# Performance work log

Hardware: AMD Instinct MI355X
Metric: run time of the kernel (lower is better)

The kernel has to match this reference:

```python
import jax, jax.numpy as jnp
import numpy as np

H = 12          # num_attention_heads
D = 768         # hidden_size
R = 4           # channel_shrink_ratio
DH = D // H     # 64, attention_head_size
DL = D // R     # 192, layout hidden size
DHL = DH // R   # 16, layout head size
NEG = jnp.finfo(jnp.float32).min


def setup_inputs() -> dict:
    key = jax.random.key(0)
    ks = jax.random.split(key, 16)
    B, S = 8, 1024
    s = 0.02
    inp = {
        "hidden_states": jax.random.normal(ks[0], (B, S, D), jnp.float32),
        "layout_hidden_states": jax.random.normal(ks[1], (B, S, DL), jnp.float32),
        "attention_mask": jnp.ones((B, S), jnp.float32),
        "Wq": jax.random.normal(ks[2], (D, D), jnp.float32) * s,
        "bq": jnp.zeros((D,), jnp.float32),
        "Wk": jax.random.normal(ks[3], (D, D), jnp.float32) * s,
        "bk": jnp.zeros((D,), jnp.float32),
        "Wv": jax.random.normal(ks[4], (D, D), jnp.float32) * s,
        "bv": jnp.zeros((D,), jnp.float32),
        "Wlq": jax.random.normal(ks[5], (DL, DL), jnp.float32) * s,
        "blq": jnp.zeros((DL,), jnp.float32),
        "Wlk": jax.random.normal(ks[6], (DL, DL), jnp.float32) * s,
        "blk": jnp.zeros((DL,), jnp.float32),
        "Wlv": jax.random.normal(ks[7], (DL, DL), jnp.float32) * s,
        "blv": jnp.zeros((DL,), jnp.float32),
    }
    return inp


def _heads(x, hd):
    # [B,S,H*hd] -> [B,H,S,hd]
    B, S, _ = x.shape
    return x.reshape(B, S, H, hd).transpose(0, 2, 1, 3)


def reference(hidden_states, layout_hidden_states, attention_mask,
              Wq, bq, Wk, bk, Wv, bv, Wlq, blq, Wlk, blk, Wlv, blv):
    B, S, _ = hidden_states.shape
    q = _heads(hidden_states @ Wq.T + bq, DH)
    k = _heads(hidden_states @ Wk.T + bk, DH)
    v = _heads(hidden_states @ Wv.T + bv, DH)
    lq = _heads(layout_hidden_states @ Wlq.T + blq, DHL)
    lk = _heads(layout_hidden_states @ Wlk.T + blk, DHL)
    lv = _heads(layout_hidden_states @ Wlv.T + blv, DHL)

    scores = jnp.einsum('bhqd,bhkd->bhqk', q, k) / jnp.sqrt(jnp.float32(DH))
    lscores = jnp.einsum('bhqd,bhkd->bhqk', lq, lk) / jnp.sqrt(jnp.float32(DHL))
    fused = scores + lscores  # cross-added scores (same for both streams)

    bias = (1.0 - attention_mask)[:, None, None, :] * NEG  # [B,1,1,S]
    fused = fused + bias

    probs = jax.nn.softmax(fused, axis=-1)   # dropout disabled (p=0)

    ctx = jnp.einsum('bhqk,bhkd->bhqd', probs, v)
    ctx = ctx.transpose(0, 2, 1, 3).reshape(B, S, D)
    lctx = jnp.einsum('bhqk,bhkd->bhqd', probs, lv)
    lctx = lctx.transpose(0, 2, 1, 3).reshape(B, S, DL)
    return ctx, lctx, probs
```

## Files before the change

kernel.cpp:

```cpp
#include <hip/hip_runtime.h>

#define NH   12
#define SEQ  1024
#define NB   8
#define DCAT 96
#define DV   80

typedef __attribute__((ext_vector_type(8))) short  bf16x8;
typedef __attribute__((ext_vector_type(4))) float  f32x4;
typedef __attribute__((ext_vector_type(4))) unsigned short u16x4;

static __device__ __forceinline__ unsigned short f2bf(float x) {
    unsigned int u = __float_as_uint(x);
    u += 0x7fffu + ((u >> 16) & 1u);
    return (unsigned short)(u >> 16);
}
static __device__ __forceinline__ f32x4 fzero() {
    f32x4 z; z[0]=0.f; z[1]=0.f; z[2]=0.f; z[3]=0.f; return z;
}
static __device__ __forceinline__ unsigned int cvtpk(float lo, float hi) {
    unsigned int r;
    asm("v_cvt_pk_bf16_f32 %0, %1, %2" : "=v"(r) : "v"(lo), "v"(hi));
    return r;
}

#define GLDS16(gp, lp) __builtin_amdgcn_global_load_lds(                      \
    (const __attribute__((address_space(1))) void*)(gp),                      \
    (__attribute__((address_space(3))) void*)(lp), 16, 0, 0)

#define WAITV(nstr) asm volatile("s_waitcnt vmcnt(" nstr ")" ::: "memory")
#define SBARRIER() do {                                                       \
    __builtin_amdgcn_sched_barrier(0);                                        \
    asm volatile("" ::: "memory");                                            \
    __builtin_amdgcn_s_barrier();                                             \
    asm volatile("" ::: "memory");                                            \
    __builtin_amdgcn_sched_barrier(0);                                        \
} while (0)

__global__ __launch_bounds__(256) void cvt_all(
    const float* __restrict__ hs, const float* __restrict__ lhs,
    const float* __restrict__ Wq, const float* __restrict__ Wk, const float* __restrict__ Wv,
    const float* __restrict__ Wlq, const float* __restrict__ Wlk, const float* __restrict__ Wlv,
    unsigned short* __restrict__ hid16, unsigned short* __restrict__ lay16,
    unsigned short* __restrict__ wqkv16, unsigned short* __restrict__ wl16)
{
    int i = blockIdx.x * 256 + threadIdx.x;
    const float* src; unsigned short* dst; int off;
    if      (i < 1572864) { src = hs;  dst = hid16;           off = i; }
    else if (i < 1966080) { src = lhs; dst = lay16;           off = i - 1572864; }
    else if (i < 2113536) { src = Wq;  dst = wqkv16;          off = i - 1966080; }
    else if (i < 2260992) { src = Wk;  dst = wqkv16 + 589824; off = i - 2113536; }
    else if (i < 2408448) { src = Wv;  dst = wqkv16 + 1179648;off = i - 2260992; }
    else if (i < 2417664) { src = Wlq; dst = wl16;            off = i - 2408448; }
    else if (i < 2426880) { src = Wlk; dst = wl16 + 36864;    off = i - 2417664; }
    else if (i < 2436096) { src = Wlv; dst = wl16 + 73728;    off = i - 2426880; }
    else return;
    f32x4 v = ((const f32x4*)src)[off];
    u16x4 o;
    o[0] = f2bf(v[0]); o[1] = f2bf(v[1]); o[2] = f2bf(v[2]); o[3] = f2bf(v[3]);
    ((u16x4*)dst)[off] = o;
}

__global__ __launch_bounds__(256) void proj_gemm(
    const unsigned short* __restrict__ A,
    const unsigned short* __restrict__ Bw,
    const float* __restrict__ b0, const float* __restrict__ b1, const float* __restrict__ b2,
    unsigned short* __restrict__ Qc, unsigned short* __restrict__ Kc, unsigned short* __restrict__ VT,
    int K, int Ntot, int variant)
{
    __shared__ __align__(16) unsigned short As[4096];
    __shared__ __align__(16) unsigned short Bs[4096];
    const int tid = threadIdx.x, w = tid >> 6, lane = tid & 63;
    const int g = lane >> 4, c = lane & 15;
    const int m0 = blockIdx.x * 128, n0 = blockIdx.y * 128;
    const int wr = w >> 1, wc = w & 1;
    const int srow = lane >> 2, scol = (lane & 3) * 8;

    f32x4 acc[4][4];
    #pragma unroll
    for (int m = 0; m < 4; m++)
        #pragma unroll
        for (int n = 0; n < 4; n++) acc[m][n] = fzero();

    const int ch0 = w * 2, ch1 = w * 2 + 1;
    const size_t arow0 = (size_t)(m0 + ch0 * 16 + srow) * K + scol;
    const size_t arow1 = (size_t)(m0 + ch1 * 16 + srow) * K + scol;
    int bn0 = n0 + ch0 * 16 + srow; if (bn0 >= Ntot) bn0 = Ntot - 1;
    int bn1 = n0 + ch1 * 16 + srow; if (bn1 >= Ntot) bn1 = Ntot - 1;
    const size_t brow0 = (size_t)bn0 * K + scol;
    const size_t brow1 = (size_t)bn1 * K + scol;

    for (int k0 = 0; k0 < K; k0 += 32) {
        __syncthreads();
        GLDS16(A  + arow0 + k0, As + ch0 * 512);
        GLDS16(A  + arow1 + k0, As + ch1 * 512);
        GLDS16(Bw + brow0 + k0, Bs + ch0 * 512);
        GLDS16(Bw + brow1 + k0, Bs + ch1 * 512);
        __syncthreads();
        bf16x8 af[4], bfr[4];
        #pragma unroll
        for (int m = 0; m < 4; m++) af[m]  = *(const bf16x8*)&As[(wr*64 + m*16 + c)*32 + g*8];
        #pragma unroll
        for (int n = 0; n < 4; n++) bfr[n] = *(const bf16x8*)&Bs[(wc*64 + n*16 + c)*32 + g*8];
        #pragma unroll
        for (int m = 0; m < 4; m++)
            #pragma unroll
            for (int n = 0; n < 4; n++)
                acc[m][n] = __builtin_amdgcn_mfma_f32_16x16x32_bf16(af[m], bfr[n], acc[m][n], 0, 0, 0);
    }

    const int b_ = m0 >> 10;
    #pragma unroll
    for (int nf = 0; nf < 4; nf++) {
        int n = n0 + wc * 64 + nf * 16 + c;
        if (n >= Ntot) continue;
        int seg, nn;
        if (variant == 0) { seg = (n >= 1536) ? 2 : ((n >= 768) ? 1 : 0); nn = n - seg * 768; }
        else              { seg = (n >= 384)  ? 2 : ((n >= 192) ? 1 : 0); nn = n - seg * 192; }
        const float* bp = (seg == 0) ? b0 : ((seg == 1) ? b1 : b2);
        float bv = bp[nn];
        float scale = (seg == 0) ? (variant ? 0.25f : 0.125f) : 1.0f;
        int h, d;
        if (variant == 0) { h = nn >> 6; d = nn & 63; }
        else              { h = nn >> 4; d = 64 + (nn & 15); }
        #pragma unroll
        for (int m = 0; m < 4; m++) {
            int row = m0 + wr * 64 + m * 16 + 4 * g;
            int s = row & 1023;
            if (seg < 2) {
                unsigned short* dst = (seg == 0) ? Qc : Kc;
                size_t base = (size_t)(b_ * NH + h) * SEQ;
                #pragma unroll
                for (int r = 0; r < 4; r++) {
                    dst[(base + s + r) * DCAT + d] = f2bf((acc[m][nf][r] + bv) * scale);
                    if (variant == 1)
                        dst[(base + s + r) * DCAT + d + 16] = 0;
                }
            } else {
                u16x4 pk;
                #pragma unroll
                for (int r = 0; r < 4; r++) pk[r] = f2bf(acc[m][nf][r] + bv);
                int kb = s >> 5, ko = s & 31;
                *(u16x4*)&VT[(((size_t)(b_ * NH + h) * 32 + kb) * DV + d) * 32 + ko] = pk;
            }
        }
    }
}

__global__ __launch_bounds__(256, 3) void attn_kernel(
    const unsigned short* __restrict__ Qc,
    const unsigned short* __restrict__ Kc,
    const unsigned short* __restrict__ VT,
    const float* __restrict__ mask,
    float* __restrict__ ctx,
    float* __restrict__ lctx,
    float* __restrict__ probs)
{
    __shared__ __align__(16) unsigned short Ks[2 * 6144];
    __shared__ __align__(16) unsigned short pbuf[4][32][36];

    const int tid = threadIdx.x, w = tid >> 6, lane = tid & 63;
    const int g = lane >> 4, c = lane & 15;

    const int bid = blockIdx.x;
    const int xc = bid & 7, j = bid >> 3;
    const int bh = xc + 8 * (j >> 3);
    const int qt = j & 7;
    const int b = bh / NH, h = bh % NH;
    const int qrb = qt * 128 + w * 32;
    const float NEGF = -3.4028234663852886e38f;

    bf16x8 qa0, qa1, qa2, qb0, qb1, qb2;
    {
        const unsigned short* qr0 = &Qc[((size_t)bh * SEQ + qrb + c) * DCAT + g * 8];
        qa0 = *(const bf16x8*)(qr0);
        qa1 = *(const bf16x8*)(qr0 + 32);
        qa2 = *(const bf16x8*)(qr0 + 64);
        const unsigned short* qr1 = qr0 + 16 * DCAT;
        qb0 = *(const bf16x8*)(qr1);
        qb1 = *(const bf16x8*)(qr1 + 32);
        qb2 = *(const bf16x8*)(qr1 + 64);
    }
    const unsigned short* Kb = Kc + (size_t)bh * SEQ * DCAT;
    const unsigned short* Vb = VT + (size_t)bh * 32 * DV * 32;
    const float* mk = mask + b * SEQ;

    const int slot8 = (g ^ ((c >> 1) & 3)) * 8;

    const unsigned short* gsrc[3]; int gstep[3];
    #pragma unroll
    for (int r = 0; r < 3; r++) {
        const int m = tid + 256 * r;
        if (m < 384) {
            int p = m >> 7, row = (m >> 2) & 31, jj = m & 3;
            int jx = jj ^ ((row >> 1) & 3);
            gsrc[r]  = Kb + row * DCAT + p * 32 + jx * 8;
            gstep[r] = 32 * DCAT;
        } else if (m < 704) {
            int mv = m - 384;
            int df = mv >> 6, cc = (mv >> 2) & 15, jj = mv & 3;
            int jx = jj ^ ((cc >> 1) & 3);
            gsrc[r]  = Vb + (df * 16 + cc) * 32 + jx * 8;
            gstep[r] = DV * 32;
        } else {
            gsrc[r]  = Vb;
            gstep[r] = 0;
        }
    }
    const int dub = w * 512;

    f32x4 cacc0[5], cacc1[5];
    #pragma unroll
    for (int nf = 0; nf < 5; nf++) { cacc0[nf] = fzero(); cacc1[nf] = fzero(); }
    float sm0 = 0.f, sm1 = 0.f;

    #pragma unroll
    for (int r = 0; r < 3; r++)
        GLDS16(gsrc[r], Ks + r * 2048 + dub);
    __builtin_amdgcn_sched_barrier(0);

    for (int t = 0; t < 32; t++) {
        const int buf = t & 1;
        if (t == 0) WAITV("0");
        else        WAITV("2");
        SBARRIER();
        if (t < 31) {
            #pragma unroll
            for (int r = 0; r < 3; r++)
                GLDS16(gsrc[r] + (t + 1) * gstep[r], Ks + (buf ^ 1) * 6144 + r * 2048 + dub);
            __builtin_amdgcn_sched_barrier(0);
        }

        #pragma unroll
        for (int ktl = 0; ktl < 2; ktl++) {
            const int rb = buf * 6144 + (ktl * 16 + c) * 32 + slot8;
            bf16x8 k0 = *(const bf16x8*)&Ks[rb];
            bf16x8 k1 = *(const bf16x8*)&Ks[rb + 1024];
            bf16x8 k2 = *(const bf16x8*)&Ks[rb + 2048];
            f32x4 m4 = *(const f32x4*)&mk[t * 32 + ktl * 16 + 4 * g];
            __builtin_amdgcn_s_setprio(1);
            f32x4 a0 = __builtin_amdgcn_mfma_f32_16x16x32_bf16(k0, qa0, fzero(), 0, 0, 0);
            f32x4 a1 = __builtin_amdgcn_mfma_f32_16x16x32_bf16(k1, qa1, fzero(), 0, 0, 0);
            f32x4 a2 = __builtin_amdgcn_mfma_f32_16x16x32_bf16(k2, qa2, fzero(), 0, 0, 0);
            f32x4 b0 = __builtin_amdgcn_mfma_f32_16x16x32_bf16(k0, qb0, fzero(), 0, 0, 0);
            f32x4 b1 = __builtin_amdgcn_mfma_f32_16x16x32_bf16(k1, qb1, fzero(), 0, 0, 0);
            f32x4 b2 = __builtin_amdgcn_mfma_f32_16x16x32_bf16(k2, qb2, fzero(), 0, 0, 0);
            __builtin_amdgcn_s_setprio(0);
            f32x4 e0, e1;
            #pragma unroll
            for (int r = 0; r < 4; r++) {
                float bias = (1.0f - m4[r]) * NEGF;
                e0[r] = __expf(a0[r] + a1[r] + a2[r] + bias);
                e1[r] = __expf(b0[r] + b1[r] + b2[r] + bias);
                sm0 += e0[r];
                sm1 += e1[r];
            }
            uint2 hh0, hh1;
            hh0.x = cvtpk(e0[0], e0[1]); hh0.y = cvtpk(e0[2], e0[3]);
            hh1.x = cvtpk(e1[0], e1[1]); hh1.y = cvtpk(e1[2], e1[3]);
            *(uint2*)&pbuf[w][c][ktl * 16 + 4 * g]      = hh0;
            *(uint2*)&pbuf[w][16 + c][ktl * 16 + 4 * g] = hh1;
        }
        const int vb0 = buf * 6144 + 3072 + c * 32 + slot8;
        bf16x8 vf0 = *(const bf16x8*)&Ks[vb0];
        bf16x8 vf1 = *(const bf16x8*)&Ks[vb0 + 512];
        bf16x8 vf2 = *(const bf16x8*)&Ks[vb0 + 1024];
        bf16x8 vf3 = *(const bf16x8*)&Ks[vb0 + 1536];
        bf16x8 vf4 = *(const bf16x8*)&Ks[vb0 + 2048];
        bf16x8 pa0 = *(const bf16x8*)&pbuf[w][c][g * 8];
        bf16x8 pa1 = *(const bf16x8*)&pbuf[w][16 + c][g * 8];
        __builtin_amdgcn_s_setprio(1);
        cacc0[0] = __builtin_amdgcn_mfma_f32_16x16x32_bf16(pa0, vf0, cacc0[0], 0, 0, 0);
        cacc1[0] = __builtin_amdgcn_mfma_f32_16x16x32_bf16(pa1, vf0, cacc1[0], 0, 0, 0);
        cacc0[1] = __builtin_amdgcn_mfma_f32_16x16x32_bf16(pa0, vf1, cacc0[1], 0, 0, 0);
        cacc1[1] = __builtin_amdgcn_mfma_f32_16x16x32_bf16(pa1, vf1, cacc1[1], 0, 0, 0);
        cacc0[2] = __builtin_amdgcn_mfma_f32_16x16x32_bf16(pa0, vf2, cacc0[2], 0, 0, 0);
        cacc1[2] = __builtin_amdgcn_mfma_f32_16x16x32_bf16(pa1, vf2, cacc1[2], 0, 0, 0);
        cacc0[3] = __builtin_amdgcn_mfma_f32_16x16x32_bf16(pa0, vf3, cacc0[3], 0, 0, 0);
        cacc1[3] = __builtin_amdgcn_mfma_f32_16x16x32_bf16(pa1, vf3, cacc1[3], 0, 0, 0);
        cacc0[4] = __builtin_amdgcn_mfma_f32_16x16x32_bf16(pa0, vf4, cacc0[4], 0, 0, 0);
        cacc1[4] = __builtin_amdgcn_mfma_f32_16x16x32_bf16(pa1, vf4, cacc1[4], 0, 0, 0);
        __builtin_amdgcn_s_setprio(0);
    }

    sm0 += __shfl_xor(sm0, 16); sm0 += __shfl_xor(sm0, 32);
    sm1 += __shfl_xor(sm1, 16); sm1 += __shfl_xor(sm1, 32);
    const float rinv0 = 1.0f / fmaxf(sm0, 1e-38f);
    const float rinv1 = 1.0f / fmaxf(sm1, 1e-38f);

    float rl0[4], rl1[4];
    #pragma unroll
    for (int r = 0; r < 4; r++) {
        rl0[r] = __shfl(rinv0, 4 * g + r);
        rl1[r] = __shfl(rinv1, 4 * g + r);
    }

    #pragma unroll
    for (int nf = 0; nf < 4; nf++)
        #pragma unroll
        for (int r = 0; r < 4; r++) {
            int q0 = qrb + 4 * g + r;
            ctx[((size_t)(b * SEQ + q0)) * 768 + h * 64 + nf * 16 + c] = cacc0[nf][r] * rl0[r];
            ctx[((size_t)(b * SEQ + q0 + 16)) * 768 + h * 64 + nf * 16 + c] = cacc1[nf][r] * rl1[r];
        }
    #pragma unroll
    for (int r = 0; r < 4; r++) {
        int q0 = qrb + 4 * g + r;
        lctx[((size_t)(b * SEQ + q0)) * 192 + h * 16 + c] = cacc0[4][r] * rl0[r];
        lctx[((size_t)(b * SEQ + q0 + 16)) * 192 + h * 16 + c] = cacc1[4][r] * rl1[r];
    }

    const int srow   = lane >> 2;
    const int schunk = (lane & 3) ^ ((lane >> 3) & 3);
    const int ssrcA  = (w * 16 + srow) * DCAT + schunk * 8;
    unsigned short* sdstA = &Ks[w * 512];

    const size_t prow0 = ((size_t)bh * SEQ + qrb + c) * SEQ;
    const size_t prow1 = prow0 + 16 * SEQ;

    SBARRIER();
    #pragma unroll
    for (int p = 0; p < 3; p++) GLDS16(Kb + ssrcA + p * 32, sdstA + p * 2048);
    __builtin_amdgcn_sched_barrier(0);

    for (int t = 0; t < 16; t++) {
        const int buf = t & 1;
        if (t == 0) WAITV("0");
        else        WAITV("12");
        SBARRIER();
        if (t < 15) {
            const unsigned short* src = Kb + (t + 1) * 6144 + ssrcA;
            unsigned short* dst = sdstA + (buf ^ 1) * 6144;
            #pragma unroll
            for (int p = 0; p < 3; p++) GLDS16(src + p * 32, dst + p * 2048);
            __builtin_amdgcn_sched_barrier(0);
        }
        #pragma unroll
        for (int ktl = 0; ktl < 4; ktl++) {
            const int rb = buf * 6144 + (ktl * 16 + c) * 32 + slot8;
            bf16x8 k0 = *(const bf16x8*)&Ks[rb];
            bf16x8 k1 = *(const bf16x8*)&Ks[rb + 2048];
            bf16x8 k2 = *(const bf16x8*)&Ks[rb + 4096];
            f32x4 m4 = *(const f32x4*)&mk[t * 64 + ktl * 16 + 4 * g];
            __builtin_amdgcn_s_setprio(1);
            f32x4 a0 = __builtin_amdgcn_mfma_f32_16x16x32_bf16(k0, qa0, fzero(), 0, 0, 0);
            f32x4 a1 = __builtin_amdgcn_mfma_f32_16x16x32_bf16(k1, qa1, fzero(), 0, 0, 0);
            f32x4 a2 = __builtin_amdgcn_mfma_f32_16x16x32_bf16(k2, qa2, fzero(), 0, 0, 0);
            f32x4 b0 = __builtin_amdgcn_mfma_f32_16x16x32_bf16(k0, qb0, fzero(), 0, 0, 0);
            f32x4 b1 = __builtin_amdgcn_mfma_f32_16x16x32_bf16(k1, qb1, fzero(), 0, 0, 0);
            f32x4 b2 = __builtin_amdgcn_mfma_f32_16x16x32_bf16(k2, qb2, fzero(), 0, 0, 0);
            __builtin_amdgcn_s_setprio(0);
            f32x4 p0, p1;
            #pragma unroll
            for (int r = 0; r < 4; r++) {
                float bias = (1.0f - m4[r]) * NEGF;
                p0[r] = __expf(a0[r] + a1[r] + a2[r] + bias) * rinv0;
                p1[r] = __expf(b0[r] + b1[r] + b2[r] + bias) * rinv1;
            }
            *(f32x4*)&probs[prow0 + (t * 64 + ktl * 16) + 4 * g] = p0;
            *(f32x4*)&probs[prow1 + (t * 64 + ktl * 16) + 4 * g] = p1;
        }
    }
}

extern "C" void kernel_launch(void* const* d_in, const int* in_sizes, int n_in,
                              void* d_out, int out_size, void* d_ws, size_t ws_size,
                              hipStream_t stream)
{
    const float* hs   = (const float*)d_in[0];
    const float* lhs  = (const float*)d_in[1];
    const float* mask = (const float*)d_in[2];
    const float* Wq   = (const float*)d_in[3];
    const float* bq   = (const float*)d_in[4];
    const float* Wk   = (const float*)d_in[5];
    const float* bk   = (const float*)d_in[6];
    const float* Wv   = (const float*)d_in[7];
    const float* bv   = (const float*)d_in[8];
    const float* Wlq  = (const float*)d_in[9];
    const float* blq  = (const float*)d_in[10];
    const float* Wlk  = (const float*)d_in[11];
    const float* blk_ = (const float*)d_in[12];
    const float* Wlv  = (const float*)d_in[13];
    const float* blv  = (const float*)d_in[14];

    float* out   = (float*)d_out;
    float* ctx   = out;
    float* lctx  = out + (size_t)NB * SEQ * 768;
    float* probs = out + (size_t)NB * SEQ * 768 + (size_t)NB * SEQ * 192;

    char* ws = (char*)d_ws;
    unsigned short* Qc     = (unsigned short*)(ws);
    unsigned short* Kc     = (unsigned short*)(ws + 18874368);
    unsigned short* VT     = (unsigned short*)(ws + 37748736);
    unsigned short* hid16  = (unsigned short*)(ws + 53477376);
    unsigned short* lay16  = (unsigned short*)(ws + 66060288);
    unsigned short* wqkv16 = (unsigned short*)(ws + 69206016);
    unsigned short* wl16   = (unsigned short*)(ws + 72744960);

    cvt_all<<<dim3(9516), dim3(256), 0, stream>>>(hs, lhs, Wq, Wk, Wv, Wlq, Wlk, Wlv,
                                                  hid16, lay16, wqkv16, wl16);

    proj_gemm<<<dim3(64, 18), dim3(256), 0, stream>>>(hid16, wqkv16, bq, bk, bv,
                                                      Qc, Kc, VT, 768, 2304, 0);
    proj_gemm<<<dim3(64, 5),  dim3(256), 0, stream>>>(lay16, wl16, blq, blk_, blv,
                                                      Qc, Kc, VT, 192, 576, 1);

    attn_kernel<<<dim3(768), dim3(256), 0, stream>>>(Qc, Kc, VT, mask, ctx, lctx, probs);
}
```

Measured before the change: 236.6 us.

## Merge projection GEMM launches and read K directly from global in probs pass

Combines the two projection GEMM launches into one grid, with blockIdx.y choosing the hidden or layout variant, which removes a kernel launch and lets both run concurrently. In the attention kernel's second pass, which recomputes scores to write normalized probabilities, the double-buffered LDS staging of K tiles with barriers is replaced by direct per-lane global loads of K rows. This drops synchronisation and LDS traffic but relies on cache hits for repeated K reads and loses explicit prefetch overlap.

```diff
diff --git a/kernel.cpp b/kernel.cpp
--- a/kernel.cpp
+++ b/kernel.cpp
@@ -62,17 +62,30 @@
 }
 
 __global__ __launch_bounds__(256) void proj_gemm(
-    const unsigned short* __restrict__ A,
-    const unsigned short* __restrict__ Bw,
-    const float* __restrict__ b0, const float* __restrict__ b1, const float* __restrict__ b2,
-    unsigned short* __restrict__ Qc, unsigned short* __restrict__ Kc, unsigned short* __restrict__ VT,
-    int K, int Ntot, int variant)
+    const unsigned short* __restrict__ Ahid,
+    const unsigned short* __restrict__ Alay,
+    const unsigned short* __restrict__ Bwqkv,
+    const unsigned short* __restrict__ Bwl,
+    const float* __restrict__ bq, const float* __restrict__ bk, const float* __restrict__ bv,
+    const float* __restrict__ blq, const float* __restrict__ blk_, const float* __restrict__ blv,
+    unsigned short* __restrict__ Qc, unsigned short* __restrict__ Kc, unsigned short* __restrict__ VT)
 {
     __shared__ __align__(16) unsigned short As[4096];
     __shared__ __align__(16) unsigned short Bs[4096];
     const int tid = threadIdx.x, w = tid >> 6, lane = tid & 63;
     const int g = lane >> 4, c = lane & 15;
-    const int m0 = blockIdx.x * 128, n0 = blockIdx.y * 128;
+
+    const int variant = (blockIdx.y < 18) ? 0 : 1;
+    const unsigned short* A  = variant ? Alay : Ahid;
+    const unsigned short* Bw = variant ? Bwl  : Bwqkv;
+    const float* b0 = variant ? blq  : bq;
+    const float* b1 = variant ? blk_ : bk;
+    const float* b2 = variant ? blv  : bv;
+    const int K    = variant ? 192 : 768;
+    const int Ntot = variant ? 576 : 2304;
+    const int m0 = blockIdx.x * 128;
+    const int n0 = (variant ? (blockIdx.y - 18) : blockIdx.y) * 128;
+
     const int wr = w >> 1, wc = w & 1;
     const int srow = lane >> 2, scol = (lane & 3) * 8;
 
@@ -310,56 +323,34 @@
         lctx[((size_t)(b * SEQ + q0 + 16)) * 192 + h * 16 + c] = cacc1[4][r] * rl1[r];
     }
 
-    const int srow   = lane >> 2;
-    const int schunk = (lane & 3) ^ ((lane >> 3) & 3);
-    const int ssrcA  = (w * 16 + srow) * DCAT + schunk * 8;
-    unsigned short* sdstA = &Ks[w * 512];
-
     const size_t prow0 = ((size_t)bh * SEQ + qrb + c) * SEQ;
     const size_t prow1 = prow0 + 16 * SEQ;
-
-    SBARRIER();
-    #pragma unroll
-    for (int p = 0; p < 3; p++) GLDS16(Kb + ssrcA + p * 32, sdstA + p * 2048);
-    __builtin_amdgcn_sched_barrier(0);
-
-    for (int t = 0; t < 16; t++) {
-        const int buf = t & 1;
-        if (t == 0) WAITV("0");
-        else        WAITV("12");
-        SBARRIER();
-        if (t < 15) {
-            const unsigned short* src = Kb + (t + 1) * 6144 + ssrcA;
-            unsigned short* dst = sdstA + (buf ^ 1) * 6144;
-            #pragma unroll
-            for (int p = 0; p < 3; p++) GLDS16(src + p * 32, dst + p * 2048);
-            __builtin_amdgcn_sched_barrier(0);
-        }
-        #pragma unroll
-        for (int ktl = 0; ktl < 4; ktl++) {
-            const int rb = buf * 6144 + (ktl * 16 + c) * 32 + slot8;
-            bf16x8 k0 = *(const bf16x8*)&Ks[rb];
-            bf16x8 k1 = *(const bf16x8*)&Ks[rb + 2048];
-            bf16x8 k2 = *(const bf16x8*)&Ks[rb + 4096];
-            f32x4 m4 = *(const f32x4*)&mk[t * 64 + ktl * 16 + 4 * g];
-            __builtin_amdgcn_s_setprio(1);
-            f32x4 a0 = __builtin_amdgcn_mfma_f32_16x16x32_bf16(k0, qa0, fzero(), 0, 0, 0);
-            f32x4 a1 = __builtin_amdgcn_mfma_f32_16x16x32_bf16(k1, qa1, fzero(), 0, 0, 0);
-            f32x4 a2 = __builtin_amdgcn_mfma_f32_16x16x32_bf16(k2, qa2, fzero(), 0, 0, 0);
-            f32x4 b0 = __builtin_amdgcn_mfma_f32_16x16x32_bf16(k0, qb0, fzero(), 0, 0, 0);
-            f32x4 b1 = __builtin_amdgcn_mfma_f32_16x16x32_bf16(k1, qb1, fzero(), 0, 0, 0);
-            f32x4 b2 = __builtin_amdgcn_mfma_f32_16x16x32_bf16(k2, qb2, fzero(), 0, 0, 0);
-            __builtin_amdgcn_s_setprio(0);
-            f32x4 p0, p1;
-            #pragma unroll
-            for (int r = 0; r < 4; r++) {
-                float bias = (1.0f - m4[r]) * NEGF;
-                p0[r] = __expf(a0[r] + a1[r] + a2[r] + bias) * rinv0;
-                p1[r] = __expf(b0[r] + b1[r] + b2[r] + bias) * rinv1;
-            }
-            *(f32x4*)&probs[prow0 + (t * 64 + ktl * 16) + 4 * g] = p0;
-            *(f32x4*)&probs[prow1 + (t * 64 + ktl * 16) + 4 * g] = p1;
-        }
+    const unsigned short* KbG = Kb + g * 8;
+
+    #pragma unroll 2
+    for (int kt = 0; kt < 64; kt++) {
+        const unsigned short* kr = KbG + (size_t)(kt * 16 + c) * DCAT;
+        bf16x8 k0 = *(const bf16x8*)(kr);
+        bf16x8 k1 = *(const bf16x8*)(kr + 32);
+        bf16x8 k2 = *(const bf16x8*)(kr + 64);
+        f32x4 m4 = *(const f32x4*)&mk[kt * 16 + 4 * g];
+        __builtin_amdgcn_s_setprio(1);
+        f32x4 a0 = __builtin_amdgcn_mfma_f32_16x16x32_bf16(k0, qa0, fzero(), 0, 0, 0);
+        f32x4 a1 = __builtin_amdgcn_mfma_f32_16x16x32_bf16(k1, qa1, fzero(), 0, 0, 0);
+        f32x4 a2 = __builtin_amdgcn_mfma_f32_16x16x32_bf16(k2, qa2, fzero(), 0, 0, 0);
+        f32x4 b0 = __builtin_amdgcn_mfma_f32_16x16x32_bf16(k0, qb0, fzero(), 0, 0, 0);
+        f32x4 b1 = __builtin_amdgcn_mfma_f32_16x16x32_bf16(k1, qb1, fzero(), 0, 0, 0);
+        f32x4 b2 = __builtin_amdgcn_mfma_f32_16x16x32_bf16(k2, qb2, fzero(), 0, 0, 0);
+        __builtin_amdgcn_s_setprio(0);
+        f32x4 p0, p1;
+        #pragma unroll
+        for (int r = 0; r < 4; r++) {
+            float bias = (1.0f - m4[r]) * NEGF;
+            p0[r] = __expf(a0[r] + a1[r] + a2[r] + bias) * rinv0;
+            p1[r] = __expf(b0[r] + b1[r] + b2[r] + bias) * rinv1;
+        }
+        *(f32x4*)&probs[prow0 + kt * 16 + 4 * g] = p0;
+        *(f32x4*)&probs[prow1 + kt * 16 + 4 * g] = p1;
     }
 }
 
@@ -400,10 +391,9 @@
     cvt_all<<<dim3(9516), dim3(256), 0, stream>>>(hs, lhs, Wq, Wk, Wv, Wlq, Wlk, Wlv,
                                                   hid16, lay16, wqkv16, wl16);
 
-    proj_gemm<<<dim3(64, 18), dim3(256), 0, stream>>>(hid16, wqkv16, bq, bk, bv,
-                                                      Qc, Kc, VT, 768, 2304, 0);
-    proj_gemm<<<dim3(64, 5),  dim3(256), 0, stream>>>(lay16, wl16, blq, blk_, blv,
-                                                      Qc, Kc, VT, 192, 576, 1);
+    proj_gemm<<<dim3(64, 23), dim3(256), 0, stream>>>(hid16, lay16, wqkv16, wl16,
+                                                      bq, bk, bv, blq, blk_, blv,
+                                                      Qc, Kc, VT);
 
     attn_kernel<<<dim3(768), dim3(256), 0, stream>>>(Qc, Kc, VT, mask, ctx, lctx, probs);
 }
```

Result: slower. 262.1 us (+10.8%).
